# Kernel tuning notes

Measured on AMD Instinct MI355X. Metric: run time of the kernel, lower is better.

Reference implementation:

```python
import jax, jax.numpy as jnp
import numpy as np

N = 8000        # nodes
E = 64000       # directed edges (before self-loops)
F_IN = 3201     # node_dim=1 + encoding_dim(128)*25
N_TRAIN = 4000


def setup_inputs() -> dict:
    key = jax.random.key(0)
    k = jax.random.split(key, 4)
    d = {
        'x': jax.random.normal(k[0], (N, F_IN), dtype=jnp.float32),
        'edge_index': jax.random.randint(k[1], (2, E), 0, N),
        'y': jax.random.uniform(k[2], (N,), dtype=jnp.float32),
        'train_idx': jax.random.randint(k[3], (N_TRAIN,), 0, N),
    }
    cnt = [0]
    def w(shape, fan_in):
        cnt[0] += 1
        kk = jax.random.fold_in(jax.random.key(1), cnt[0])
        return (jax.random.normal(kk, shape, dtype=jnp.float32) / np.float32(np.sqrt(fan_in)))
    ones = lambda n: jnp.ones((n,), jnp.float32)
    zeros = lambda n: jnp.zeros((n,), jnp.float32)
    d['bn0_g'] = ones(F_IN); d['bn0_b'] = zeros(F_IN)
    d['W1l'] = w((F_IN, 1024), F_IN); d['W1r'] = w((F_IN, 1024), F_IN)
    d['a1'] = w((2, 512), 512); d['b1'] = zeros(1024)
    d['bn1_g'] = ones(1024); d['bn1_b'] = zeros(1024)
    d['W2l'] = w((1024, 512), 1024); d['W2r'] = w((1024, 512), 1024)
    d['a2'] = w((1, 512), 512); d['b2'] = zeros(512)
    d['bn2_g'] = ones(512); d['bn2_b'] = zeros(512)
    d['W3l'] = w((512, 512), 512); d['W3r'] = w((512, 512), 512)
    d['a3'] = w((1, 512), 512); d['b3'] = zeros(512)
    d['bn3_g'] = ones(512); d['bn3_b'] = zeros(512)
    d['W4l'] = w((512, 512), 512); d['W4r'] = w((512, 512), 512)
    d['a4'] = w((1, 512), 512); d['b4'] = zeros(512)
    d['Wh'] = w((512, 1), 512); d['bh'] = zeros(1)
    return d


def _batchnorm(h, g, b, eps=1e-5):
    # training-mode batch statistics over the node dim
    m = h.mean(axis=0)
    v = h.var(axis=0)
    return (h - m) * jax.lax.rsqrt(v + jnp.float32(eps)) * g + b


def _gatv2(h, src, dst, Wl, Wr, att, bias, n):
    # GATv2Conv with concat heads, softmax over incoming edges, aggr='mean'
    H, C = att.shape
    xl = (h @ Wl).reshape(n, H, C)   # source transform
    xr = (h @ Wr).reshape(n, H, C)   # target transform
    z = jax.nn.leaky_relu(xl[src] + xr[dst], negative_slope=0.2)  # [E,H,C]
    e = jnp.einsum('ehc,hc->eh', z, att)                          # [E,H]
    emax = jax.ops.segment_max(e, dst, num_segments=n)            # segment softmax
    ex = jnp.exp(e - emax[dst])
    denom = jax.ops.segment_sum(ex, dst, num_segments=n)
    alpha = ex / denom[dst]
    agg = jax.ops.segment_sum(alpha[:, :, None] * xl[src], dst, num_segments=n)
    deg = jax.ops.segment_sum(jnp.ones(src.shape[0], h.dtype), dst, num_segments=n)
    return (agg / deg[:, None, None]).reshape(n, H * C) + bias


def reference(x, edge_index, y, train_idx, bn0_g, bn0_b, W1l, W1r, a1, b1,
              bn1_g, bn1_b, W2l, W2r, a2, b2, bn2_g, bn2_b, W3l, W3r, a3, b3,
              bn3_g, bn3_b, W4l, W4r, a4, b4, Wh, bh):
    n = x.shape[0]
    loops = jnp.arange(n, dtype=edge_index.dtype)  # PyG add_self_loops=True
    src = jnp.concatenate([edge_index[0], loops])
    dst = jnp.concatenate([edge_index[1], loops])
    h = _batchnorm(x, bn0_g, bn0_b)
    h = _gatv2(h, src, dst, W1l, W1r, a1, b1, n)          # -> [N,1024]
    h = jax.nn.relu(_batchnorm(h, bn1_g, bn1_b))
    h = _gatv2(h, src, dst, W2l, W2r, a2, b2, n)          # -> [N,512]
    h = jax.nn.relu(_batchnorm(h, bn2_g, bn2_b))
    h = _gatv2(h, src, dst, W3l, W3r, a3, b3, n)
    h = jax.nn.relu(_batchnorm(h, bn3_g, bn3_b))
    h = jax.nn.relu(_gatv2(h, src, dst, W4l, W4r, a4, b4, n))
    pred = jax.nn.sigmoid(h @ Wh + bh)[:, 0]              # [N]
    return pred[train_idx], y[train_idx]
```

## Files before the change

### kernel.cpp

```cpp
#include <hip/hip_runtime.h>
#include <math.h>

typedef __bf16 bf16x8 __attribute__((ext_vector_type(8)));
typedef float f32x4 __attribute__((ext_vector_type(4)));
typedef unsigned short ushort8 __attribute__((ext_vector_type(8)));

__device__ __forceinline__ float bf2f(unsigned short u) {
  union { unsigned int i; float f; } c; c.i = ((unsigned int)u) << 16; return c.f;
}
__device__ __forceinline__ unsigned short f2bf(float f) {
  union { float f; unsigned int i; } c; c.f = f;
  unsigned int r = (c.i + 0x7fffu + ((c.i >> 16) & 1u)) >> 16;
  return (unsigned short)r;
}

__global__ void zero_k(float* __restrict__ statz, int nz, int* __restrict__ deg, int n) {
  int i = blockIdx.x * blockDim.x + threadIdx.x;
  if (i < nz) statz[i] = 0.f;
  if (i < n) deg[i] = 1;
}

__global__ void deg_count_k(const int* __restrict__ dst, int* __restrict__ deg, int e) {
  int i = blockIdx.x * blockDim.x + threadIdx.x;
  if (i < e) atomicAdd(&deg[dst[i]], 1);
}

__global__ void scan_k(const int* __restrict__ deg, int* __restrict__ offsets,
                       int* __restrict__ cursor, int n) {
  __shared__ int sums[1024];
  int tid = threadIdx.x;
  int chunk = (n + 1023) >> 10;
  int base = tid * chunk;
  int s = 0;
  for (int i = 0; i < chunk; ++i) {
    int j = base + i;
    if (j < n) s += deg[j];
  }
  sums[tid] = s;
  __syncthreads();
  for (int off = 1; off < 1024; off <<= 1) {
    int v = (tid >= off) ? sums[tid - off] : 0;
    __syncthreads();
    sums[tid] += v;
    __syncthreads();
  }
  int run = sums[tid] - s;
  for (int i = 0; i < chunk; ++i) {
    int j = base + i;
    if (j < n) {
      offsets[j] = run;
      cursor[j] = run;
      run += deg[j];
    }
  }
  if (tid == 1023) offsets[n] = sums[1023];
}

__global__ void csr_fill_k(const int* __restrict__ src, const int* __restrict__ dst,
                           int* __restrict__ cursor, int* __restrict__ csr_src,
                           int e, int n) {
  int i = blockIdx.x * blockDim.x + threadIdx.x;
  if (i >= e + n) return;
  int s, d;
  if (i < e) { s = src[i]; d = dst[i]; }
  else       { s = i - e;  d = s; }
  int pos = atomicAdd(&cursor[d], 1);
  csr_src[pos] = s;
}

__global__ __launch_bounds__(256)
void stats_convert_k(const float* __restrict__ x, unsigned short* __restrict__ Abf,
                     float* __restrict__ P1, float* __restrict__ P2,
                     int M, int K, int Kp) {
  int c = blockIdx.x * 256 + threadIdx.x;
  if (c >= Kp) return;
  int rows = (M + gridDim.y - 1) / gridDim.y;
  int r0 = blockIdx.y * rows;
  int r1 = min(M, r0 + rows);
  if (c >= K) {
    for (int r = r0; r < r1; ++r) Abf[(size_t)r * Kp + c] = 0;
    return;
  }
  float a = 0.f, b = 0.f;
  int r = r0;
  for (; r + 4 <= r1; r += 4) {
    float v0 = x[(size_t)(r + 0) * K + c];
    float v1 = x[(size_t)(r + 1) * K + c];
    float v2 = x[(size_t)(r + 2) * K + c];
    float v3 = x[(size_t)(r + 3) * K + c];
    a += v0 + v1 + v2 + v3;
    b += v0 * v0 + v1 * v1 + v2 * v2 + v3 * v3;
    Abf[(size_t)(r + 0) * Kp + c] = f2bf(v0);
    Abf[(size_t)(r + 1) * Kp + c] = f2bf(v1);
    Abf[(size_t)(r + 2) * Kp + c] = f2bf(v2);
    Abf[(size_t)(r + 3) * Kp + c] = f2bf(v3);
  }
  for (; r < r1; ++r) {
    float v = x[(size_t)r * K + c];
    a += v; b += v * v;
    Abf[(size_t)r * Kp + c] = f2bf(v);
  }
  P1[(size_t)blockIdx.y * Kp + c] = a;
  P2[(size_t)blockIdx.y * Kp + c] = b;
}

__global__ __launch_bounds__(256)
void col_stats_bf_k(const unsigned short* __restrict__ h, int M, int D,
                    float* __restrict__ P1, float* __restrict__ P2) {
  int c = blockIdx.x * 256 + threadIdx.x;
  if (c >= D) return;
  int rows = (M + gridDim.y - 1) / gridDim.y;
  int r0 = blockIdx.y * rows;
  int r1 = min(M, r0 + rows);
  float a = 0.f, b = 0.f;
  int r = r0;
  for (; r + 4 <= r1; r += 4) {
    float v0 = bf2f(h[(size_t)(r + 0) * D + c]);
    float v1 = bf2f(h[(size_t)(r + 1) * D + c]);
    float v2 = bf2f(h[(size_t)(r + 2) * D + c]);
    float v3 = bf2f(h[(size_t)(r + 3) * D + c]);
    a += v0 + v1 + v2 + v3;
    b += v0 * v0 + v1 * v1 + v2 * v2 + v3 * v3;
  }
  for (; r < r1; ++r) {
    float v = bf2f(h[(size_t)r * D + c]);
    a += v; b += v * v;
  }
  P1[(size_t)blockIdx.y * D + c] = a;
  P2[(size_t)blockIdx.y * D + c] = b;
}

__global__ __launch_bounds__(256)
void coef_k(const float* __restrict__ P1, const float* __restrict__ P2,
            const float* __restrict__ g, const float* __restrict__ b,
            float* __restrict__ outA, float* __restrict__ outC,
            int K, int Kp, int ny, float invM) {
  int cc = threadIdx.x & 63;
  int c = blockIdx.x * 64 + cc;
  int yl = threadIdx.x >> 6;
  __shared__ float red[2][4][64];
  float s1 = 0.f, s2 = 0.f;
  if (c < Kp) {
#pragma unroll 4
    for (int y = yl; y < ny; y += 4) {
      s1 += P1[(size_t)y * Kp + c];
      s2 += P2[(size_t)y * Kp + c];
    }
  }
  red[0][yl][cc] = s1;
  red[1][yl][cc] = s2;
  __syncthreads();
  if (yl == 0 && c < Kp) {
    s1 = red[0][0][cc] + red[0][1][cc] + red[0][2][cc] + red[0][3][cc];
    s2 = red[1][0][cc] + red[1][1][cc] + red[1][2][cc] + red[1][3][cc];
    if (c >= K) { outA[c] = 0.f; outC[c] = 0.f; return; }
    float m = s1 * invM;
    float var = fmaxf(s2 * invM - m * m, 0.f);
    float a = rsqrtf(var + 1e-5f) * g[c];
    outA[c] = a;
    outC[c] = b[c] - m * a;
  }
}

__global__ __launch_bounds__(256)
void bn_apply8_k(const unsigned short* __restrict__ h,
                 const float* __restrict__ aC, const float* __restrict__ cC,
                 unsigned short* __restrict__ outb, size_t total, int D) {
  size_t i = ((size_t)blockIdx.x * 256 + threadIdx.x) * 8;
  if (i >= total) return;
  ushort8 u = *(const ushort8*)(h + i);
  int c = (int)(i % (size_t)D);
  ushort8 o;
#pragma unroll
  for (int j = 0; j < 8; ++j) {
    float v = bf2f(u[j]) * aC[c + j] + cC[c + j];
    o[j] = f2bf(fmaxf(v, 0.f));
  }
  *(ushort8*)(outb + i) = o;
}

__global__ __launch_bounds__(256)
void wconv_pair_k(const float* __restrict__ Wl, const float* __restrict__ Wr,
                  unsigned short* __restrict__ WT, int K, int N, int Kp,
                  const float* __restrict__ coefA) {
  const float* W = blockIdx.z ? Wr : Wl;
  unsigned short* WTo = WT + (size_t)blockIdx.z * N * Kp;
  __shared__ float t[32][33];
  int n0 = blockIdx.x * 32, k0 = blockIdx.y * 32;
  int tx = threadIdx.x & 31, ty = threadIdx.x >> 5;
#pragma unroll
  for (int i = 0; i < 32; i += 8) {
    int k = k0 + ty + i, nn = n0 + tx;
    float v = (k < K && nn < N) ? W[(size_t)k * N + nn] : 0.f;
    t[ty + i][tx] = v;
  }
  float ascale = 1.f;
  if (coefA) {
    int k = k0 + tx;
    ascale = (k < Kp) ? coefA[k] : 0.f;
  }
  __syncthreads();
#pragma unroll
  for (int i = 0; i < 32; i += 8) {
    int nn = n0 + ty + i, k = k0 + tx;
    if (nn < N && k < Kp) {
      WTo[(size_t)nn * Kp + k] = f2bf(t[tx][ty + i] * ascale);
    }
  }
}

__global__ __launch_bounds__(256)
void bias_fold_k(const float* __restrict__ Wl, const float* __restrict__ Wr,
                 const float* __restrict__ coefC, float* __restrict__ bias,
                 int K, int N, int KCH) {
  int col = blockIdx.x * 256 + threadIdx.x;
  if (col >= 2 * N) return;
  const float* W = (col >= N) ? Wr : Wl;
  int nn = (col >= N) ? col - N : col;
  int k0 = blockIdx.y * KCH;
  int k1 = min(K, k0 + KCH);
  float s = 0.f;
  int k = k0;
#pragma unroll 8
  for (; k + 8 <= k1; k += 8) {
    s = fmaf(coefC[k + 0], W[(size_t)(k + 0) * N + nn], s);
    s = fmaf(coefC[k + 1], W[(size_t)(k + 1) * N + nn], s);
    s = fmaf(coefC[k + 2], W[(size_t)(k + 2) * N + nn], s);
    s = fmaf(coefC[k + 3], W[(size_t)(k + 3) * N + nn], s);
    s = fmaf(coefC[k + 4], W[(size_t)(k + 4) * N + nn], s);
    s = fmaf(coefC[k + 5], W[(size_t)(k + 5) * N + nn], s);
    s = fmaf(coefC[k + 6], W[(size_t)(k + 6) * N + nn], s);
    s = fmaf(coefC[k + 7], W[(size_t)(k + 7) * N + nn], s);
  }
  for (; k < k1; ++k) s = fmaf(coefC[k], W[(size_t)k * N + nn], s);
  atomicAdd(&bias[col], s);
}

template <int BMT>
__global__ __launch_bounds__(512, 2)
void gemm256_k(const unsigned short* __restrict__ A,
               const unsigned short* __restrict__ Bt,
               unsigned short* __restrict__ outL, unsigned short* __restrict__ outR,
               const float* __restrict__ bias, int M, int Nh, int K) {
  constexpr int MF = BMT / 32;
  constexpr int SA = (BMT * 8) / 512;
  constexpr int SB = 4;
  __shared__ unsigned short sA[2][BMT * 64];
  __shared__ unsigned short sB[2][256 * 64];
  const int tid = threadIdx.x;
  const int wave = tid >> 6, lane = tid & 63;
  const int wm = wave >> 2, wn = wave & 3;
  const int l16 = lane & 15, l4 = lane >> 4;

  int nwg = gridDim.x * gridDim.y;
  int bid = blockIdx.y * gridDim.x + blockIdx.x;
  int q = nwg >> 3, r8 = nwg & 7;
  int xcd = bid & 7, ord = bid >> 3;
  int swz = (xcd < r8 ? xcd * (q + 1) : r8 * (q + 1) + (xcd - r8) * q) + ord;
  int bx = swz % gridDim.x, by = swz / gridDim.x;
  const int row0 = by * BMT, col0 = bx * 256;
  const int NT = K >> 6;

  f32x4 acc[MF][4] = {};

  auto stage = [&](int t, int b) {
    int kt = t << 6;
#pragma unroll
    for (int i = 0; i < SA; ++i) {
      int slot = i * 512 + tid;
      int r = slot >> 3;
      int g = (slot & 7) ^ (r & 7);
      int ra = row0 + r; ra = ra < M ? ra : M - 1;
      const unsigned short* ga = A + (size_t)ra * K + kt + g * 8;
      __builtin_amdgcn_global_load_lds(
          (const __attribute__((address_space(1))) void*)ga,
          (__attribute__((address_space(3))) void*)&sA[b][slot * 8], 16, 0, 0);
    }
#pragma unroll
    for (int i = 0; i < SB; ++i) {
      int slot = i * 512 + tid;
      int r = slot >> 3;
      int g = (slot & 7) ^ (r & 7);
      const unsigned short* gb = Bt + (size_t)(col0 + r) * K + kt + g * 8;
      __builtin_amdgcn_global_load_lds(
          (const __attribute__((address_space(1))) void*)gb,
          (__attribute__((address_space(3))) void*)&sB[b][slot * 8], 16, 0, 0);
    }
  };

  stage(0, 0);
  if (NT > 1) stage(1, 1);
  if constexpr (BMT == 256) asm volatile("s_waitcnt vmcnt(8)" ::: "memory");
  else                      asm volatile("s_waitcnt vmcnt(6)" ::: "memory");
  __builtin_amdgcn_sched_barrier(0);
  __builtin_amdgcn_s_barrier();

  int cur = 0;
  for (int t = 0; t < NT; ++t) {
#pragma unroll
    for (int s = 0; s < 2; ++s) {
      bf16x8 afr[MF], bfr[4];
#pragma unroll
      for (int i = 0; i < MF; ++i) {
        int rl = wm * (BMT / 2) + i * 16 + l16;
        int g = s * 4 + l4;
        afr[i] = *(const bf16x8*)&sA[cur][rl * 64 + ((g ^ (rl & 7)) << 3)];
      }
#pragma unroll
      for (int j = 0; j < 4; ++j) {
        int rl = wn * 64 + j * 16 + l16;
        int g = s * 4 + l4;
        bfr[j] = *(const bf16x8*)&sB[cur][rl * 64 + ((g ^ (rl & 7)) << 3)];
      }
      __builtin_amdgcn_s_setprio(1);
#pragma unroll
      for (int i = 0; i < MF; ++i)
#pragma unroll
        for (int j = 0; j < 4; ++j)
          acc[i][j] = __builtin_amdgcn_mfma_f32_16x16x32_bf16(afr[i], bfr[j], acc[i][j], 0, 0, 0);
      __builtin_amdgcn_s_setprio(0);
    }
    if (t + 1 == NT) break;
    __builtin_amdgcn_s_barrier();
    if (t + 2 < NT) {
      stage(t + 2, cur);
      if constexpr (BMT == 256) asm volatile("s_waitcnt vmcnt(8)" ::: "memory");
      else                      asm volatile("s_waitcnt vmcnt(6)" ::: "memory");
    } else {
      asm volatile("s_waitcnt vmcnt(0)" ::: "memory");
    }
    __builtin_amdgcn_sched_barrier(0);
    __builtin_amdgcn_s_barrier();
    cur ^= 1;
  }

#pragma unroll
  for (int i = 0; i < MF; ++i) {
#pragma unroll
    for (int j = 0; j < 4; ++j) {
      int col = col0 + wn * 64 + j * 16 + l16;
      float bv = bias ? bias[col] : 0.f;
      unsigned short* base; int cc;
      if (col < Nh) { base = outL; cc = col; }
      else          { base = outR; cc = col - Nh; }
      int rb = row0 + wm * (BMT / 2) + i * 16 + l4 * 4;
#pragma unroll
      for (int r = 0; r < 4; ++r) {
        int rr = rb + r;
        if (rr < M) base[(size_t)rr * Nh + cc] = f2bf(acc[i][j][r] + bv);
      }
    }
  }
}

template <int H>
__global__ __launch_bounds__(256)
void gat_edge_k(const unsigned short* __restrict__ xl, const unsigned short* __restrict__ xr,
                const float* __restrict__ att, const float* __restrict__ bias,
                const int* __restrict__ csr, const int* __restrict__ offsets,
                unsigned short* __restrict__ out, int n, int relu) {
  int gw = (blockIdx.x * 256 + threadIdx.x) >> 6;
  int lane = threadIdx.x & 63;
  if (gw >= n * H) return;
  int node, head;
  if (H == 1) { node = gw; head = 0; }
  else        { node = gw >> 1; head = gw & 1; }
  const int W = H * 512;
  const size_t rowoff = (size_t)node * W + head * 512;
  const size_t choff = (size_t)head * 512 + (size_t)(lane * 8);

  float xrv[8], atv[8];
  {
    ushort8 u = *(const ushort8*)(xr + rowoff + lane * 8);
    const float* ap = att + head * 512 + lane * 8;
#pragma unroll
    for (int j = 0; j < 8; ++j) { xrv[j] = bf2f(u[j]); atv[j] = ap[j]; }
  }
  int p0 = offsets[node], p1 = offsets[node + 1];
  ushort8 u0 = *(const ushort8*)(xl + (size_t)csr[p0] * W + choff);
  ushort8 u1 = u0, u2 = u0;
  if (p0 + 1 < p1) u1 = *(const ushort8*)(xl + (size_t)csr[p0 + 1] * W + choff);
  if (p0 + 2 < p1) u2 = *(const ushort8*)(xl + (size_t)csr[p0 + 2] * W + choff);

  float m = -1e30f, l = 0.f;
  float acc[8];
#pragma unroll
  for (int j = 0; j < 8; ++j) acc[j] = 0.f;
  for (int p = p0; p < p1; ++p) {
    ushort8 u = u0;
    u0 = u1; u1 = u2;
    if (p + 3 < p1) u2 = *(const ushort8*)(xl + (size_t)csr[p + 3] * W + choff);
    float lv[8];
    float e = 0.f;
#pragma unroll
    for (int j = 0; j < 8; ++j) {
      lv[j] = bf2f(u[j]);
      float z = lv[j] + xrv[j];
      z = fmaxf(z, 0.f) + 0.2f * fminf(z, 0.f);
      e = fmaf(z, atv[j], e);
    }
#pragma unroll
    for (int off = 32; off > 0; off >>= 1) e += __shfl_xor(e, off, 64);
    float mn = fmaxf(m, e);
    float corr = __expf(m - mn);
    float w = __expf(e - mn);
    l = l * corr + w;
#pragma unroll
    for (int j = 0; j < 8; ++j) acc[j] = acc[j] * corr + w * lv[j];
    m = mn;
  }
  float inv = 1.f / (l * (float)(p1 - p0));
  const float* bp = bias + head * 512 + lane * 8;
  ushort8 o;
#pragma unroll
  for (int j = 0; j < 8; ++j) {
    float v = acc[j] * inv + bp[j];
    if (relu) v = fmaxf(v, 0.f);
    o[j] = f2bf(v);
  }
  *(ushort8*)(out + rowoff + lane * 8) = o;
}

__global__ void head_gather_k(const unsigned short* __restrict__ h, const float* __restrict__ Wh,
                   const float* __restrict__ bh, const float* __restrict__ y,
                   const int* __restrict__ tidx, float* __restrict__ out, int nt) {
  int gw = (blockIdx.x * 256 + threadIdx.x) >> 6;
  int lane = threadIdx.x & 63;
  if (gw >= nt) return;
  int j = tidx[gw];
  ushort8 u = *(const ushort8*)(h + (size_t)j * 512 + lane * 8);
  const float* wp = Wh + lane * 8;
  float s = 0.f;
#pragma unroll
  for (int q = 0; q < 8; ++q) s = fmaf(bf2f(u[q]), wp[q], s);
#pragma unroll
  for (int off = 32; off > 0; off >>= 1) s += __shfl_xor(s, off, 64);
  if (lane == 0) {
    out[gw] = 1.f / (1.f + __expf(-(s + bh[0])));
    out[nt + gw] = y[j];
  }
}

extern "C" void kernel_launch(void* const* d_in, const int* in_sizes, int n_in,
                              void* d_out, int out_size, void* d_ws, size_t ws_size,
                              hipStream_t stream) {
  const float* x     = (const float*)d_in[0];
  const int*   ei    = (const int*)d_in[1];
  const float* y     = (const float*)d_in[2];
  const int*   tidx  = (const int*)d_in[3];
  const float* bn0_g = (const float*)d_in[4];
  const float* bn0_b = (const float*)d_in[5];
  const float* W1l   = (const float*)d_in[6];
  const float* W1r   = (const float*)d_in[7];
  const float* a1    = (const float*)d_in[8];
  const float* b1    = (const float*)d_in[9];
  const float* bn1_g = (const float*)d_in[10];
  const float* bn1_b = (const float*)d_in[11];
  const float* W2l   = (const float*)d_in[12];
  const float* W2r   = (const float*)d_in[13];
  const float* a2    = (const float*)d_in[14];
  const float* b2    = (const float*)d_in[15];
  const float* bn2_g = (const float*)d_in[16];
  const float* bn2_b = (const float*)d_in[17];
  const float* W3l   = (const float*)d_in[18];
  const float* W3r   = (const float*)d_in[19];
  const float* a3    = (const float*)d_in[20];
  const float* b3    = (const float*)d_in[21];
  const float* bn3_g = (const float*)d_in[22];
  const float* bn3_b = (const float*)d_in[23];
  const float* W4l   = (const float*)d_in[24];
  const float* W4r   = (const float*)d_in[25];
  const float* a4    = (const float*)d_in[26];
  const float* b4    = (const float*)d_in[27];
  const float* Wh    = (const float*)d_in[28];
  const float* bh    = (const float*)d_in[29];
  float* out = (float*)d_out;

  const int n   = in_sizes[2];
  const int E   = in_sizes[1] / 2;
  const int FIN = in_sizes[4];
  const int NT  = in_sizes[3];
  const int ET  = E + n;
  const int KP1 = 3264;
  const int NY0 = 200;
  const int NYS = 160;

  unsigned short* us = (unsigned short*)d_ws;
  const size_t ABF_SZ = (size_t)n * KP1;
  unsigned short* Abf = us;
  unsigned short* hb  = us + ABF_SZ;
  unsigned short* xlb = hb + (size_t)n * 1024;
  unsigned short* xrb = xlb + (size_t)n * 1024;
  float* fp = (float*)(xrb + (size_t)n * 1024);
  float* biasb = fp;           fp += 2048;
  float* coefA = fp;           fp += 3328;
  float* coefC = fp;           fp += 3328;
  float* aC    = fp;           fp += 1024;
  float* cC    = fp;           fp += 1024;
  int* deg     = (int*)fp;
  int* offsets = deg + n;
  int* cursor  = offsets + n + 1;
  int* csr     = cursor + n;
  unsigned short* W1T = hb;
  unsigned short* WT  = Abf + (size_t)n * 1024;
  float* P0a = (float*)hb;
  float* P0b = P0a + (size_t)NY0 * KP1;
  float* Psa = (float*)(Abf + (size_t)n * 1024 + 8ull * 1024 * 1024);
  float* Psb = Psa + (size_t)NYS * 1024;

  const int kZeroCount = 2048;
  int zmax = n > kZeroCount ? n : kZeroCount;
  zero_k<<<(zmax + 255) / 256, 256, 0, stream>>>(biasb, kZeroCount, deg, n);
  deg_count_k<<<(E + 255) / 256, 256, 0, stream>>>(ei + E, deg, E);
  scan_k<<<1, 1024, 0, stream>>>(deg, offsets, cursor, n);
  csr_fill_k<<<(ET + 255) / 256, 256, 0, stream>>>(ei, ei + E, cursor, csr, E, n);

  float invM = 1.f / (float)n;

  {
    dim3 g((KP1 + 255) / 256, NY0);
    stats_convert_k<<<g, 256, 0, stream>>>(x, Abf, P0a, P0b, n, FIN, KP1);
    coef_k<<<(KP1 + 63) / 64, 256, 0, stream>>>(P0a, P0b, bn0_g, bn0_b,
                                                coefA, coefC, FIN, KP1, NY0, invM);
  }

  {
    dim3 gw1(1024 / 32, KP1 / 32, 2);
    wconv_pair_k<<<gw1, 256, 0, stream>>>(W1l, W1r, W1T, FIN, 1024, KP1, coefA);
    dim3 gb(8, (FIN + 127) / 128);
    bias_fold_k<<<gb, 256, 0, stream>>>(W1l, W1r, coefC, biasb, FIN, 1024, 128);
    dim3 g(2048 / 256, (n + 255) / 256);
    gemm256_k<256><<<g, 512, 0, stream>>>(Abf, W1T, xlb, xrb, biasb, n, 1024, KP1);
  }
  gat_edge_k<2><<<(n * 2 + 3) / 4, 256, 0, stream>>>(xlb, xrb, a1, b1, csr, offsets, hb, n, 0);
  {
    dim3 g(1024 / 256, NYS);
    col_stats_bf_k<<<g, 256, 0, stream>>>(hb, n, 1024, Psa, Psb);
    coef_k<<<1024 / 64, 256, 0, stream>>>(Psa, Psb, bn1_g, bn1_b, aC, cC, 1024, 1024, NYS, invM);
    bn_apply8_k<<<(int)(((size_t)n * 1024 / 8 + 255) / 256), 256, 0, stream>>>(
        hb, aC, cC, Abf, (size_t)n * 1024, 1024);
  }

  {
    dim3 gw2(512 / 32, 1024 / 32, 2);
    wconv_pair_k<<<gw2, 256, 0, stream>>>(W2l, W2r, WT, 1024, 512, 1024, nullptr);
    dim3 g(1024 / 256, (n + 127) / 128);
    gemm256_k<128><<<g, 512, 0, stream>>>(Abf, WT, xlb, xrb, nullptr, n, 512, 1024);
  }
  gat_edge_k<1><<<(n + 3) / 4, 256, 0, stream>>>(xlb, xrb, a2, b2, csr, offsets, hb, n, 0);
  {
    dim3 g(512 / 256, NYS);
    col_stats_bf_k<<<g, 256, 0, stream>>>(hb, n, 512, Psa, Psb);
    coef_k<<<512 / 64, 256, 0, stream>>>(Psa, Psb, bn2_g, bn2_b, aC, cC, 512, 512, NYS, invM);
    bn_apply8_k<<<(int)(((size_t)n * 512 / 8 + 255) / 256), 256, 0, stream>>>(
        hb, aC, cC, Abf, (size_t)n * 512, 512);
  }

  {
    dim3 gw3(512 / 32, 512 / 32, 2);
    wconv_pair_k<<<gw3, 256, 0, stream>>>(W3l, W3r, WT, 512, 512, 512, nullptr);
    dim3 g(1024 / 256, (n + 127) / 128);
    gemm256_k<128><<<g, 512, 0, stream>>>(Abf, WT, xlb, xrb, nullptr, n, 512, 512);
  }
  gat_edge_k<1><<<(n + 3) / 4, 256, 0, stream>>>(xlb, xrb, a3, b3, csr, offsets, hb, n, 0);
  {
    dim3 g(512 / 256, NYS);
    col_stats_bf_k<<<g, 256, 0, stream>>>(hb, n, 512, Psa, Psb);
    coef_k<<<512 / 64, 256, 0, stream>>>(Psa, Psb, bn3_g, bn3_b, aC, cC, 512, 512, NYS, invM);
    bn_apply8_k<<<(int)(((size_t)n * 512 / 8 + 255) / 256), 256, 0, stream>>>(
        hb, aC, cC, Abf, (size_t)n * 512, 512);
  }

  {
    dim3 gw4(512 / 32, 512 / 32, 2);
    wconv_pair_k<<<gw4, 256, 0, stream>>>(W4l, W4r, WT, 512, 512, 512, nullptr);
    dim3 g(1024 / 256, (n + 127) / 128);
    gemm256_k<128><<<g, 512, 0, stream>>>(Abf, WT, xlb, xrb, nullptr, n, 512, 512);
  }
  gat_edge_k<1><<<(n + 3) / 4, 256, 0, stream>>>(xlb, xrb, a4, b4, csr, offsets, hb, n, 1);

  head_gather_k<<<(NT + 3) / 4, 256, 0, stream>>>(hb, Wh, bh, y, tidx, out, NT);
}
```

Before: 722.0 us.

## Switch GEMM to triple-buffered K=32 LDS pipeline with single barrier per step

```diff
diff --git a/kernel.cpp b/kernel.cpp
--- a/kernel.cpp
+++ b/kernel.cpp
@@ -243,10 +243,10 @@
                unsigned short* __restrict__ outL, unsigned short* __restrict__ outR,
                const float* __restrict__ bias, int M, int Nh, int K) {
   constexpr int MF = BMT / 32;
-  constexpr int SA = (BMT * 8) / 512;
-  constexpr int SB = 4;
-  __shared__ unsigned short sA[2][BMT * 64];
-  __shared__ unsigned short sB[2][256 * 64];
+  constexpr int LA = BMT / 128;
+  constexpr int LB = 2;
+  __shared__ unsigned short sA[3][BMT * 32];
+  __shared__ unsigned short sB[3][256 * 32];
   const int tid = threadIdx.x;
   const int wave = tid >> 6, lane = tid & 63;
   const int wm = wave >> 2, wn = wave & 3;
@@ -259,29 +259,31 @@
   int swz = (xcd < r8 ? xcd * (q + 1) : r8 * (q + 1) + (xcd - r8) * q) + ord;
   int bx = swz % gridDim.x, by = swz / gridDim.x;
   const int row0 = by * BMT, col0 = bx * 256;
-  const int NT = K >> 6;
+  const int NT = K >> 5;
 
   f32x4 acc[MF][4] = {};
 
   auto stage = [&](int t, int b) {
-    int kt = t << 6;
-#pragma unroll
-    for (int i = 0; i < SA; ++i) {
+    int kt = t << 5;
+#pragma unroll
+    for (int i = 0; i < LA; ++i) {
       int slot = i * 512 + tid;
-      int r = slot >> 3;
-      int g = (slot & 7) ^ (r & 7);
-      int ra = row0 + r; ra = ra < M ? ra : M - 1;
+      int line = slot >> 3;
+      int row = line * 2 + ((slot >> 2) & 1);
+      int g = (slot & 3) ^ (line & 3);
+      int ra = row0 + row; ra = ra < M ? ra : M - 1;
       const unsigned short* ga = A + (size_t)ra * K + kt + g * 8;
       __builtin_amdgcn_global_load_lds(
           (const __attribute__((address_space(1))) void*)ga,
           (__attribute__((address_space(3))) void*)&sA[b][slot * 8], 16, 0, 0);
     }
 #pragma unroll
-    for (int i = 0; i < SB; ++i) {
+    for (int i = 0; i < LB; ++i) {
       int slot = i * 512 + tid;
-      int r = slot >> 3;
-      int g = (slot & 7) ^ (r & 7);
-      const unsigned short* gb = Bt + (size_t)(col0 + r) * K + kt + g * 8;
+      int line = slot >> 3;
+      int row = line * 2 + ((slot >> 2) & 1);
+      int g = (slot & 3) ^ (line & 3);
+      const unsigned short* gb = Bt + (size_t)(col0 + row) * K + kt + g * 8;
       __builtin_amdgcn_global_load_lds(
           (const __attribute__((address_space(1))) void*)gb,
           (__attribute__((address_space(3))) void*)&sB[b][slot * 8], 16, 0, 0);
@@ -289,49 +291,47 @@
   };
 
   stage(0, 0);
-  if (NT > 1) stage(1, 1);
-  if constexpr (BMT == 256) asm volatile("s_waitcnt vmcnt(8)" ::: "memory");
-  else                      asm volatile("s_waitcnt vmcnt(6)" ::: "memory");
+  stage(1, 1);
+  if constexpr (BMT == 256) asm volatile("s_waitcnt vmcnt(4)" ::: "memory");
+  else                      asm volatile("s_waitcnt vmcnt(3)" ::: "memory");
   __builtin_amdgcn_sched_barrier(0);
   __builtin_amdgcn_s_barrier();
 
-  int cur = 0;
+  int bc = 0, bs = 2;
   for (int t = 0; t < NT; ++t) {
-#pragma unroll
-    for (int s = 0; s < 2; ++s) {
-      bf16x8 afr[MF], bfr[4];
-#pragma unroll
-      for (int i = 0; i < MF; ++i) {
-        int rl = wm * (BMT / 2) + i * 16 + l16;
-        int g = s * 4 + l4;
-        afr[i] = *(const bf16x8*)&sA[cur][rl * 64 + ((g ^ (rl & 7)) << 3)];
+    if (t + 2 < NT) stage(t + 2, bs);
+    bf16x8 afr[MF], bfr[4];
+#pragma unroll
+    for (int i = 0; i < MF; ++i) {
+      int rl = wm * (BMT / 2) + i * 16 + l16;
+      afr[i] = *(const bf16x8*)&sA[bc][(rl >> 1) * 64 + (rl & 1) * 32 +
+                                       ((l4 ^ ((rl >> 1) & 3)) << 3)];
+    }
+#pragma unroll
+    for (int j = 0; j < 4; ++j) {
+      int rl = wn * 64 + j * 16 + l16;
+      bfr[j] = *(const bf16x8*)&sB[bc][(rl >> 1) * 64 + (rl & 1) * 32 +
+                                       ((l4 ^ ((rl >> 1) & 3)) << 3)];
+    }
+    __builtin_amdgcn_s_setprio(1);
+#pragma unroll
+    for (int i = 0; i < MF; ++i)
+#pragma unroll
+      for (int j = 0; j < 4; ++j)
+        acc[i][j] = __builtin_amdgcn_mfma_f32_16x16x32_bf16(afr[i], bfr[j], acc[i][j], 0, 0, 0);
+    __builtin_amdgcn_s_setprio(0);
+    if (t + 1 < NT) {
+      if (t + 2 < NT) {
+        if constexpr (BMT == 256) asm volatile("s_waitcnt vmcnt(4)" ::: "memory");
+        else                      asm volatile("s_waitcnt vmcnt(3)" ::: "memory");
+      } else {
+        asm volatile("s_waitcnt vmcnt(0)" ::: "memory");
       }
-#pragma unroll
-      for (int j = 0; j < 4; ++j) {
-        int rl = wn * 64 + j * 16 + l16;
-        int g = s * 4 + l4;
-        bfr[j] = *(const bf16x8*)&sB[cur][rl * 64 + ((g ^ (rl & 7)) << 3)];
-      }
-      __builtin_amdgcn_s_setprio(1);
-#pragma unroll
-      for (int i = 0; i < MF; ++i)
-#pragma unroll
-        for (int j = 0; j < 4; ++j)
-          acc[i][j] = __builtin_amdgcn_mfma_f32_16x16x32_bf16(afr[i], bfr[j], acc[i][j], 0, 0, 0);
-      __builtin_amdgcn_s_setprio(0);
-    }
-    if (t + 1 == NT) break;
-    __builtin_amdgcn_s_barrier();
-    if (t + 2 < NT) {
-      stage(t + 2, cur);
-      if constexpr (BMT == 256) asm volatile("s_waitcnt vmcnt(8)" ::: "memory");
-      else                      asm volatile("s_waitcnt vmcnt(6)" ::: "memory");
-    } else {
-      asm volatile("s_waitcnt vmcnt(0)" ::: "memory");
-    }
-    __builtin_amdgcn_sched_barrier(0);
-    __builtin_amdgcn_s_barrier();
-    cur ^= 1;
+      __builtin_amdgcn_sched_barrier(0);
+      __builtin_amdgcn_s_barrier();
+    }
+    bc = bc + 1 < 3 ? bc + 1 : 0;
+    bs = bs + 1 < 3 ? bs + 1 : 0;
   }
 
 #pragma unroll
```

Result: slower. 756.3 us (+4.7%).

## Add 8-phase pipelined 256x256 GEMM for layer-1 projection

Applied to the files above, without the earlier changes.

```diff
diff --git a/kernel.cpp b/kernel.cpp
--- a/kernel.cpp
+++ b/kernel.cpp
@@ -344,6 +344,129 @@
       if (col < Nh) { base = outL; cc = col; }
       else          { base = outR; cc = col - Nh; }
       int rb = row0 + wm * (BMT / 2) + i * 16 + l4 * 4;
+#pragma unroll
+      for (int r = 0; r < 4; ++r) {
+        int rr = rb + r;
+        if (rr < M) base[(size_t)rr * Nh + cc] = f2bf(acc[i][j][r] + bv);
+      }
+    }
+  }
+}
+
+__global__ __launch_bounds__(512, 2)
+void gemm8p_k(const unsigned short* __restrict__ A,
+              const unsigned short* __restrict__ Bt,
+              unsigned short* __restrict__ outL, unsigned short* __restrict__ outR,
+              const float* __restrict__ bias, int M, int Nh, int K) {
+  __shared__ unsigned short lds[2][2][2][128 * 64];
+  const int tid = threadIdx.x;
+  const int wave = tid >> 6, lane = tid & 63;
+  const int wm = wave >> 2, wn = wave & 3;
+  const int l16 = lane & 15, l4 = lane >> 4;
+  const int row0 = blockIdx.y * 256, col0 = blockIdx.x * 256;
+  const int NT = K >> 6, NI = NT >> 1;
+
+  f32x4 acc[8][4] = {};
+  bf16x8 Bfr[4][2];
+
+  auto stageH = [&](int T, int d, int mat, int h) {
+    int kt = (T < NT ? T : NT - 1) << 6;
+    const unsigned short* base = mat ? Bt : A;
+    int r0g = mat ? col0 : row0;
+#pragma unroll
+    for (int it = 0; it < 2; ++it) {
+      int slot = it * 512 + tid;
+      int rw = slot >> 3, g = slot & 7;
+      int gr = r0g + h * 128 + rw;
+      if (!mat) gr = gr < M ? gr : M - 1;
+      const unsigned short* gp = base + (size_t)gr * K + kt + ((g ^ (rw & 7)) << 3);
+      __builtin_amdgcn_global_load_lds(
+          (const __attribute__((address_space(1))) void*)gp,
+          (__attribute__((address_space(3))) void*)&lds[d][mat][h][slot * 8], 16, 0, 0);
+    }
+  };
+  auto dsA = [&](int d, int q, bf16x8 (&Afr)[2][2]) {
+#pragma unroll
+    for (int mi = 0; mi < 2; ++mi)
+#pragma unroll
+      for (int ks = 0; ks < 2; ++ks) {
+        int rw = (2 * q + mi) * 16 + l16;
+        int g = ks * 4 + l4;
+        Afr[mi][ks] = *(const bf16x8*)&lds[d][0][wm][rw * 64 + ((g ^ (rw & 7)) << 3)];
+      }
+  };
+  auto dsB = [&](int d) {
+#pragma unroll
+    for (int j = 0; j < 4; ++j)
+#pragma unroll
+      for (int ks = 0; ks < 2; ++ks) {
+        int rl = wn * 64 + j * 16 + l16;
+        int rw = rl & 127, h = rl >> 7;
+        int g = ks * 4 + l4;
+        Bfr[j][ks] = *(const bf16x8*)&lds[d][1][h][rw * 64 + ((g ^ (rw & 7)) << 3)];
+      }
+  };
+  auto mfmaQ = [&](int q, bf16x8 (&Afr)[2][2]) {
+    __builtin_amdgcn_s_setprio(1);
+#pragma unroll
+    for (int mi = 0; mi < 2; ++mi)
+#pragma unroll
+      for (int j = 0; j < 4; ++j)
+#pragma unroll
+        for (int ks = 0; ks < 2; ++ks)
+          acc[2 * q + mi][j] = __builtin_amdgcn_mfma_f32_16x16x32_bf16(
+              Afr[mi][ks], Bfr[j][ks], acc[2 * q + mi][j], 0, 0, 0);
+    __builtin_amdgcn_s_setprio(0);
+  };
+
+  stageH(0, 0, 0, 0); stageH(0, 0, 0, 1);
+  stageH(0, 0, 1, 0); stageH(0, 0, 1, 1);
+  stageH(1, 1, 1, 0); stageH(1, 1, 1, 1);
+  asm volatile("s_waitcnt vmcnt(4)" ::: "memory");
+  __builtin_amdgcn_sched_barrier(0);
+  __builtin_amdgcn_s_barrier();
+
+  for (int i = 0; i < NI; ++i) {
+    int T1 = 2 * i + 1, T2 = 2 * i + 2, T3 = 2 * i + 3;
+    bf16x8 Afr[2][2];
+#pragma unroll
+    for (int p = 0; p < 8; ++p) {
+      int d = p >> 2;
+      int qq = p & 3;
+      if (qq == 0) dsB(d);
+      dsA(d, qq, Afr);
+      switch (p) {
+        case 0: stageH(T1, 1, 0, 0); break;
+        case 1: stageH(T1, 1, 0, 1); break;
+        case 2: stageH(T2, 0, 1, 0); break;
+        case 3: stageH(T2, 0, 1, 1); break;
+        case 4: stageH(T2, 0, 0, 0); break;
+        case 5: stageH(T2, 0, 0, 1); break;
+        case 6: stageH(T3, 1, 1, 0); break;
+        case 7: stageH(T3, 1, 1, 1); break;
+      }
+      __builtin_amdgcn_s_barrier();
+      asm volatile("s_waitcnt lgkmcnt(0)" ::: "memory");
+      __builtin_amdgcn_sched_barrier(0);
+      mfmaQ(qq, Afr);
+      if (p == 3 || p == 7) {
+        asm volatile("s_waitcnt vmcnt(4)" ::: "memory");
+        __builtin_amdgcn_sched_barrier(0);
+      }
+      __builtin_amdgcn_s_barrier();
+    }
+  }
+
+#pragma unroll
+  for (int i = 0; i < 8; ++i) {
+#pragma unroll
+    for (int j = 0; j < 4; ++j) {
+      int col = col0 + wn * 64 + j * 16 + l16;
+      float bv = bias ? bias[col] : 0.f;
+      unsigned short* base; int cc;
+      if (col < Nh) { base = outL; cc = col; }
+      else          { base = outR; cc = col - Nh; }
+      int rb = row0 + wm * 128 + i * 16 + l4 * 4;
 #pragma unroll
       for (int r = 0; r < 4; ++r) {
         int rr = rb + r;
@@ -481,7 +604,7 @@
   const int FIN = in_sizes[4];
   const int NT  = in_sizes[3];
   const int ET  = E + n;
-  const int KP1 = 3264;
+  const int KP1 = 3328;
   const int NY0 = 200;
   const int NYS = 160;
 
@@ -530,7 +653,7 @@
     dim3 gb(8, (FIN + 127) / 128);
     bias_fold_k<<<gb, 256, 0, stream>>>(W1l, W1r, coefC, biasb, FIN, 1024, 128);
     dim3 g(2048 / 256, (n + 255) / 256);
-    gemm256_k<256><<<g, 512, 0, stream>>>(Abf, W1T, xlb, xrb, biasb, n, 1024, KP1);
+    gemm8p_k<<<g, 512, 0, stream>>>(Abf, W1T, xlb, xrb, biasb, n, 1024, KP1);
   }
   gat_edge_k<2><<<(n * 2 + 3) / 4, 256, 0, stream>>>(xlb, xrb, a1, b1, csr, offsets, hb, n, 0);
   {
```

New measurement: 707.6 us. -2.0%, faster.
